# Kernel tuning notes

Hardware: AMD Instinct MI355X
Metric: run time of the kernel (lower is better)

The kernel has to match this reference:

```python
import jax, jax.numpy as jnp
import numpy as np


def _layernorm(x, g, b, eps=1e-5):
    mu = jnp.mean(x, axis=-1, keepdims=True)
    var = jnp.mean(jnp.square(x - mu), axis=-1, keepdims=True)
    return (x - mu) * jax.lax.rsqrt(var + eps) * g + b


def setup_inputs() -> dict:
    key = jax.random.key(0)
    ks = jax.random.split(key, 8)
    B, S, E, K, H = 32, 64, 768, 36, 4
    w = 0.02
    return {
        "x": jax.random.normal(ks[0], (B, S, E), dtype=jnp.float32),
        "y": jax.random.normal(ks[1], (B * S, K, E), dtype=jnp.float32),
        "ln_gamma": jnp.ones((H, E), jnp.float32),
        "ln_beta": jnp.zeros((H, E), jnp.float32),
        "W1": jax.random.normal(ks[2], (H, E, E), dtype=jnp.float32) * w,
        "b1": jnp.zeros((H, E), jnp.float32),
        "W2x": jax.random.normal(ks[3], (H, E), dtype=jnp.float32) * w,  # first half of Linear(2E,1)
        "W2y": jax.random.normal(ks[4], (H, E), dtype=jnp.float32) * w,  # second half of Linear(2E,1)
        "b2": jnp.zeros((H,), jnp.float32),
        "Wm": jax.random.normal(ks[5], (H * E, E), dtype=jnp.float32) * w,
        "bm": jnp.zeros((E,), jnp.float32),
        "select_indegree_num": 36,
    }


def reference(x, y, ln_gamma, ln_beta, W1, b1, W2x, W2y, b2, Wm, bm, select_indegree_num):
    # x: [B,S,E], y: [B*S,K,E]; dropout layers are identity in eval mode.
    B, S, E = x.shape
    H = ln_gamma.shape[0]
    xf = x.reshape(B * S, E)
    outs = []
    for h in range(H):
        # shared linear1 (LayerNorm + Linear) applied to both x and y
        x_ = _layernorm(xf, ln_gamma[h], ln_beta[h]) @ W1[h] + b1[h]          # [BS,E]
        y_ = _layernorm(y, ln_gamma[h], ln_beta[h]) @ W1[h] + b1[h]           # [BS,K,E]
        logit = (x_ @ W2x[h])[:, None] + y_ @ W2y[h] + b2[h]                  # [BS,K]
        prob = jax.nn.softmax(logit, axis=1)                                   # softmax over neighbors
        a = jnp.einsum('nk,nke->ne', prob, y_)                                 # weighted sum, [BS,E]
        outs.append(jax.nn.gelu(xf + a))                                       # GELU(x + a)
    cat = jnp.concatenate(outs, axis=-1)                                       # [BS,H*E]
    res = jax.nn.gelu(cat @ Wm + bm).reshape(B, S, E)
    return x + res  # has_residual=True
```

## Files before the change

kernel.cpp:

```cpp
#include <hip/hip_runtime.h>
#include <hip/hip_bf16.h>
#include <math.h>

#define EE 768
#define HH 4
#define KK 36
#define BSN 2048

typedef __attribute__((ext_vector_type(8))) short short8;
typedef __attribute__((ext_vector_type(4))) short short4v;
typedef __attribute__((ext_vector_type(4))) float float4v;

__device__ inline short f2bf(float x){
  return __builtin_bit_cast(short, __float2bfloat16(x));
}
__device__ inline float bf2f(short s){
  return __bfloat162float(__builtin_bit_cast(__hip_bfloat16, s));
}
__device__ inline float gelu_tanh(float x){
  float t = tanhf(0.79788456080286536f * (x + 0.044715f * x * x * x));
  return 0.5f * x * (1.0f + t);
}

__global__ __launch_bounds__(256) void k_v(const float* __restrict__ W1,
                                           const float* __restrict__ W2y,
                                           const float* __restrict__ g,
                                           const float* __restrict__ b1,
                                           float* __restrict__ v,
                                           float* __restrict__ b1p){
  const int wid  = blockIdx.x * 4 + (threadIdx.x >> 6);
  const int lane = threadIdx.x & 63;
  const int h = wid / EE, e = wid % EE;
  const float* W  = W1 + ((size_t)h * EE + e) * EE;
  const float* wy = W2y + h * EE;
  float acc = 0.f;
  #pragma unroll
  for (int j = 0; j < 12; ++j){
    int f = lane + 64 * j;
    acc += W[f] * wy[f];
  }
  #pragma unroll
  for (int off = 32; off; off >>= 1) acc += __shfl_xor(acc, off);
  if (lane == 0) v[h * EE + e] = g[h * EE + e] * acc;

  int idx = blockIdx.x * 256 + threadIdx.x;
  if (idx < HH * EE) b1p[idx] = b1[idx];
}

__global__ __launch_bounds__(256) void k_b1p_acc(const float* __restrict__ W1,
                                                 const float* __restrict__ beta,
                                                 float* __restrict__ b1p){
  const int h   = blockIdx.x >> 6;
  const int ec0 = (blockIdx.x & 63) * 12;
  const float* W  = W1 + (size_t)h * EE * EE;
  const float* bt = beta + h * EE;
  const int f = threadIdx.x;
  float a0 = 0.f, a1 = 0.f, a2 = 0.f;
  #pragma unroll
  for (int e = ec0; e < ec0 + 12; ++e){
    float be = bt[e];
    const float* row = W + (size_t)e * EE;
    a0 += be * row[f];
    a1 += be * row[f + 256];
    a2 += be * row[f + 512];
  }
  atomicAdd(&b1p[h * EE + f],       a0);
  atomicAdd(&b1p[h * EE + f + 256], a1);
  atomicAdd(&b1p[h * EE + f + 512], a2);
}

__global__ __launch_bounds__(256) void k_tW1(const float* __restrict__ W1,
                                             const float* __restrict__ g,
                                             short* __restrict__ W1t){
  __shared__ float tile[32][33];
  const int h  = blockIdx.z;
  const int e0 = blockIdx.x * 32, f0 = blockIdx.y * 32;
  const int tx = threadIdx.x & 31, ty = threadIdx.x >> 5;
  const float* W = W1 + (size_t)h * EE * EE;
  #pragma unroll
  for (int i = 0; i < 4; ++i){
    int e = e0 + ty + 8 * i;
    tile[ty + 8 * i][tx] = W[(size_t)e * EE + f0 + tx] * g[h * EE + e];
  }
  __syncthreads();
  #pragma unroll
  for (int i = 0; i < 4; ++i){
    int f = f0 + ty + 8 * i;
    W1t[((size_t)h * EE + f) * EE + e0 + tx] = f2bf(tile[tx][ty + 8 * i]);
  }
}

__global__ __launch_bounds__(256) void k_tWm(const float* __restrict__ Wm,
                                             short* __restrict__ Wmt){
  __shared__ float tile[32][33];
  const int c0 = blockIdx.x * 32, f0 = blockIdx.y * 32;
  const int tx = threadIdx.x & 31, ty = threadIdx.x >> 5;
  #pragma unroll
  for (int i = 0; i < 4; ++i){
    tile[ty + 8 * i][tx] = Wm[(size_t)(c0 + ty + 8 * i) * EE + f0 + tx];
  }
  __syncthreads();
  #pragma unroll
  for (int i = 0; i < 4; ++i){
    Wmt[(size_t)(f0 + ty + 8 * i) * (HH * EE) + c0 + tx] = f2bf(tile[tx][ty + 8 * i]);
  }
}

__global__ __launch_bounds__(256) void k_pass_y(const float* __restrict__ y,
                                                const float* __restrict__ v,
                                                short* __restrict__ p_y){
  const int wave = threadIdx.x >> 6, lane = threadIdx.x & 63;
  const int n = blockIdx.x * 4 + wave;
  const float* base = y + (size_t)n * KK * EE + 4 * lane;

  float4v vreg[HH][3];
  #pragma unroll
  for (int h = 0; h < HH; ++h)
    #pragma unroll
    for (int j = 0; j < 3; ++j)
      vreg[h][j] = *(const float4v*)(v + h * EE + 4 * lane + 256 * j);

  float4v acc[HH][3];
  #pragma unroll
  for (int h = 0; h < HH; ++h)
    #pragma unroll
    for (int j = 0; j < 3; ++j)
      acc[h][j] = (float4v){0.f, 0.f, 0.f, 0.f};
  float m[HH], l[HH];
  #pragma unroll
  for (int h = 0; h < HH; ++h){ m[h] = -INFINITY; l[h] = 0.f; }

  float4v bufA[3], bufB[3];
  #pragma unroll
  for (int j = 0; j < 3; ++j) bufA[j] = *(const float4v*)(base + 256 * j);
  #pragma unroll
  for (int j = 0; j < 3; ++j) bufB[j] = *(const float4v*)(base + EE + 256 * j);

  #pragma unroll 2
  for (int k = 0; k < KK; ++k){
    float4v cur[3];
    #pragma unroll
    for (int j = 0; j < 3; ++j) cur[j] = bufA[j];
    #pragma unroll
    for (int j = 0; j < 3; ++j) bufA[j] = bufB[j];
    if (k + 2 < KK){
      const float* rp = base + (size_t)(k + 2) * EE;
      #pragma unroll
      for (int j = 0; j < 3; ++j) bufB[j] = *(const float4v*)(rp + 256 * j);
    }

    float s = 0.f, s2 = 0.f;
    #pragma unroll
    for (int j = 0; j < 3; ++j)
      #pragma unroll
      for (int c = 0; c < 4; ++c){ float t = cur[j][c]; s += t; s2 += t * t; }
    #pragma unroll
    for (int off = 32; off; off >>= 1){
      s  += __shfl_xor(s, off);
      s2 += __shfl_xor(s2, off);
    }
    const float mu = s * (1.f / EE);
    const float rs = rsqrtf(s2 * (1.f / EE) - mu * mu + 1e-5f);

    float d[HH] = {0.f, 0.f, 0.f, 0.f};
    #pragma unroll
    for (int j = 0; j < 3; ++j)
      #pragma unroll
      for (int c = 0; c < 4; ++c){
        float t = (cur[j][c] - mu) * rs;
        cur[j][c] = t;
        d[0] += t * vreg[0][j][c];
        d[1] += t * vreg[1][j][c];
        d[2] += t * vreg[2][j][c];
        d[3] += t * vreg[3][j][c];
      }
    #pragma unroll
    for (int off = 32; off; off >>= 1){
      d[0] += __shfl_xor(d[0], off);
      d[1] += __shfl_xor(d[1], off);
      d[2] += __shfl_xor(d[2], off);
      d[3] += __shfl_xor(d[3], off);
    }

    #pragma unroll
    for (int h = 0; h < HH; ++h){
      if (d[h] > m[h]){
        float sc = __expf(m[h] - d[h]);
        l[h] *= sc;
        #pragma unroll
        for (int j = 0; j < 3; ++j)
          #pragma unroll
          for (int c = 0; c < 4; ++c) acc[h][j][c] *= sc;
        m[h] = d[h];
      }
      float w = __expf(d[h] - m[h]);
      l[h] += w;
      #pragma unroll
      for (int j = 0; j < 3; ++j)
        #pragma unroll
        for (int c = 0; c < 4; ++c) acc[h][j][c] += w * cur[j][c];
    }
  }

  #pragma unroll
  for (int h = 0; h < HH; ++h){
    const float inv = 1.f / l[h];
    #pragma unroll
    for (int j = 0; j < 3; ++j){
      short4v pk;
      #pragma unroll
      for (int c = 0; c < 4; ++c) pk[c] = f2bf(acc[h][j][c] * inv);
      *(short4v*)(p_y + ((size_t)h * BSN + n) * EE + 4 * lane + 256 * j) = pk;
    }
  }
}

template<int MODE>
__global__ __launch_bounds__(256) void k_gemm(const short* __restrict__ A,
                                              const short* __restrict__ Bt,
                                              const float* __restrict__ addv,
                                              const float* __restrict__ x,
                                              void* __restrict__ out,
                                              int Kdim, size_t strideA, size_t strideB){
  __shared__ short As[2][64][72];
  __shared__ short Bs[2][64][72];
  const int z = blockIdx.z;
  const short* Ah; const short* Bh; int kbeg, kend;
  if (MODE == 0){ Ah = A + strideA * z; Bh = Bt + strideB * z; kbeg = 0; kend = Kdim; }
  else          { Ah = A; Bh = Bt; kbeg = z * (Kdim >> 1); kend = kbeg + (Kdim >> 1); }

  const int tid = threadIdx.x;
  const int wave = tid >> 6, lane = tid & 63;
  const int quad = lane >> 4, l16 = lane & 15;
  const int m0 = blockIdx.x * 64, n0 = blockIdx.y * 64;
  const int r = tid >> 3, c8 = (tid & 7) * 8;

  float4v acc[4];
  #pragma unroll
  for (int t = 0; t < 4; ++t) acc[t] = (float4v){0.f, 0.f, 0.f, 0.f};

  const short* Ap0 = Ah + (size_t)(m0 + r) * Kdim + c8;
  const short* Ap1 = Ah + (size_t)(m0 + r + 32) * Kdim + c8;
  const short* Bp0 = Bh + (size_t)(n0 + r) * Kdim + c8;
  const short* Bp1 = Bh + (size_t)(n0 + r + 32) * Kdim + c8;

  short8 ra0 = *(const short8*)(Ap0 + kbeg);
  short8 ra1 = *(const short8*)(Ap1 + kbeg);
  short8 rb0 = *(const short8*)(Bp0 + kbeg);
  short8 rb1 = *(const short8*)(Bp1 + kbeg);
  *(short8*)(&As[0][r][c8])      = ra0;
  *(short8*)(&As[0][r + 32][c8]) = ra1;
  *(short8*)(&Bs[0][r][c8])      = rb0;
  *(short8*)(&Bs[0][r + 32][c8]) = rb1;
  if (kbeg + 64 < kend){
    ra0 = *(const short8*)(Ap0 + kbeg + 64);
    ra1 = *(const short8*)(Ap1 + kbeg + 64);
    rb0 = *(const short8*)(Bp0 + kbeg + 64);
    rb1 = *(const short8*)(Bp1 + kbeg + 64);
  }
  __syncthreads();

  int cur = 0;
  for (int k0 = kbeg; k0 < kend; k0 += 64){
    if (k0 + 64 < kend){
      const int nx = cur ^ 1;
      *(short8*)(&As[nx][r][c8])      = ra0;
      *(short8*)(&As[nx][r + 32][c8]) = ra1;
      *(short8*)(&Bs[nx][r][c8])      = rb0;
      *(short8*)(&Bs[nx][r + 32][c8]) = rb1;
      if (k0 + 128 < kend){
        ra0 = *(const short8*)(Ap0 + k0 + 128);
        ra1 = *(const short8*)(Ap1 + k0 + 128);
        rb0 = *(const short8*)(Bp0 + k0 + 128);
        rb1 = *(const short8*)(Bp1 + k0 + 128);
      }
    }
    #pragma unroll
    for (int kk = 0; kk < 64; kk += 32){
      short8 bf = *(const short8*)(&Bs[cur][16 * wave + l16][kk + quad * 8]);
      #pragma unroll
      for (int t = 0; t < 4; ++t){
        short8 af = *(const short8*)(&As[cur][16 * t + l16][kk + quad * 8]);
        acc[t] = __builtin_amdgcn_mfma_f32_16x16x32_bf16(af, bf, acc[t], 0, 0, 0);
      }
    }
    __syncthreads();
    cur ^= 1;
  }

  const int f = n0 + 16 * wave + l16;
  if (MODE == 0){
    const float add = addv[768 * z + f];
    #pragma unroll
    for (int t = 0; t < 4; ++t){
      #pragma unroll
      for (int rr = 0; rr < 4; ++rr){
        const int m = m0 + 16 * t + quad * 4 + rr;
        const float val = acc[t][rr] + add;
        const float xf = x[(size_t)m * EE + f];
        ((short*)out)[(size_t)m * (HH * EE) + 768 * z + f] = f2bf(gelu_tanh(xf + val));
      }
    }
  } else {
    float* po = (float*)out + (size_t)z * BSN * EE;
    #pragma unroll
    for (int t = 0; t < 4; ++t){
      #pragma unroll
      for (int rr = 0; rr < 4; ++rr){
        const int m = m0 + 16 * t + quad * 4 + rr;
        po[(size_t)m * EE + f] = acc[t][rr];
      }
    }
  }
}

__global__ __launch_bounds__(256) void k_ep(const float* __restrict__ part,
                                            const float* __restrict__ bm,
                                            const float* __restrict__ x,
                                            float* __restrict__ out){
  const size_t i = ((size_t)blockIdx.x * 256 + threadIdx.x) * 4;
  float4v p0 = *(const float4v*)(part + i);
  float4v p1 = *(const float4v*)(part + (size_t)BSN * EE + i);
  float4v xv = *(const float4v*)(x + i);
  float4v bv = *(const float4v*)(bm + (int)(i % EE));
  float4v o;
  #pragma unroll
  for (int c = 0; c < 4; ++c) o[c] = xv[c] + gelu_tanh(p0[c] + p1[c] + bv[c]);
  *(float4v*)(out + i) = o;
}

extern "C" void kernel_launch(void* const* d_in, const int* in_sizes, int n_in,
                              void* d_out, int out_size, void* d_ws, size_t ws_size,
                              hipStream_t stream){
  const float* x    = (const float*)d_in[0];
  const float* y    = (const float*)d_in[1];
  const float* g    = (const float*)d_in[2];
  const float* beta = (const float*)d_in[3];
  const float* W1   = (const float*)d_in[4];
  const float* b1   = (const float*)d_in[5];
  const float* W2y  = (const float*)d_in[7];
  const float* Wm   = (const float*)d_in[9];
  const float* bm   = (const float*)d_in[10];

  char* ws = (char*)d_ws;
  float* v    = (float*)(ws + 0);
  float* b1p  = (float*)(ws + 12288);
  short* W1t  = (short*)(ws + 24576);
  short* Wmt  = (short*)(ws + 4743168);
  short* p_y  = (short*)(ws + 9461760);
  short* catb = (short*)(ws + 22044672);
  float* part = (float*)(ws + 34627584);
  float* out  = (float*)d_out;

  k_v<<<dim3(768), dim3(256), 0, stream>>>(W1, W2y, g, b1, v, b1p);
  k_b1p_acc<<<dim3(256), dim3(256), 0, stream>>>(W1, beta, b1p);
  k_tW1<<<dim3(24, 24, 4), dim3(256), 0, stream>>>(W1, g, W1t);
  k_tWm<<<dim3(96, 24), dim3(256), 0, stream>>>(Wm, Wmt);
  k_pass_y<<<dim3(512), dim3(256), 0, stream>>>(y, v, p_y);
  k_gemm<0><<<dim3(32, 12, 4), dim3(256), 0, stream>>>(
      p_y, W1t, b1p, x, (void*)catb, 768, (size_t)2048 * 768, (size_t)768 * 768);
  k_gemm<1><<<dim3(32, 12, 2), dim3(256), 0, stream>>>(
      catb, Wmt, nullptr, nullptr, (void*)part, 3072, (size_t)0, (size_t)0);
  k_ep<<<dim3(1536), dim3(256), 0, stream>>>(part, bm, x, out);
}
```

Baseline: 427.4 us.

## Split neighbor softmax across two waves and fuse final epilogue into GEMM

```diff
diff --git a/kernel.cpp b/kernel.cpp
--- a/kernel.cpp
+++ b/kernel.cpp
@@ -109,9 +109,13 @@
 __global__ __launch_bounds__(256) void k_pass_y(const float* __restrict__ y,
                                                 const float* __restrict__ v,
                                                 short* __restrict__ p_y){
+  __shared__ float4v sacc[2][HH][3][64];
+  __shared__ float   sml[2][2][2][HH];
   const int wave = threadIdx.x >> 6, lane = threadIdx.x & 63;
-  const int n = blockIdx.x * 4 + wave;
-  const float* base = y + (size_t)n * KK * EE + 4 * lane;
+  const int row = wave >> 1, half = wave & 1;
+  const int n = blockIdx.x * 2 + row;
+  const int kh = 18;
+  const float* base = y + ((size_t)n * KK + half * kh) * EE + 4 * lane;
 
   float4v vreg[HH][3];
   #pragma unroll
@@ -137,13 +141,13 @@
   for (int j = 0; j < 3; ++j) bufB[j] = *(const float4v*)(base + EE + 256 * j);
 
   #pragma unroll 2
-  for (int k = 0; k < KK; ++k){
+  for (int k = 0; k < kh; ++k){
     float4v cur[3];
     #pragma unroll
     for (int j = 0; j < 3; ++j) cur[j] = bufA[j];
     #pragma unroll
     for (int j = 0; j < 3; ++j) bufA[j] = bufB[j];
-    if (k + 2 < KK){
+    if (k + 2 < kh){
       const float* rp = base + (size_t)(k + 2) * EE;
       #pragma unroll
       for (int j = 0; j < 3; ++j) bufB[j] = *(const float4v*)(rp + 256 * j);
@@ -202,15 +206,51 @@
     }
   }
 
+  if (lane == 0){
+    #pragma unroll
+    for (int h = 0; h < HH; ++h){
+      sml[row][half][0][h] = m[h];
+      sml[row][half][1][h] = l[h];
+    }
+  }
+  __syncthreads();
+
+  float escale[HH], L[HH];
   #pragma unroll
   for (int h = 0; h < HH; ++h){
-    const float inv = 1.f / l[h];
-    #pragma unroll
-    for (int j = 0; j < 3; ++j){
-      short4v pk;
-      #pragma unroll
-      for (int c = 0; c < 4; ++c) pk[c] = f2bf(acc[h][j][c] * inv);
-      *(short4v*)(p_y + ((size_t)h * BSN + n) * EE + 4 * lane + 256 * j) = pk;
+    const float mo = sml[row][half ^ 1][0][h];
+    const float lo = sml[row][half ^ 1][1][h];
+    const float M  = fmaxf(m[h], mo);
+    escale[h] = __expf(m[h] - M);
+    L[h] = l[h] * escale[h] + lo * __expf(mo - M);
+  }
+
+  if (half == 1){
+    #pragma unroll
+    for (int h = 0; h < HH; ++h)
+      #pragma unroll
+      for (int j = 0; j < 3; ++j){
+        float4v sv;
+        #pragma unroll
+        for (int c = 0; c < 4; ++c) sv[c] = acc[h][j][c] * escale[h];
+        sacc[row][h][j][lane] = sv;
+      }
+  }
+  __syncthreads();
+
+  if (half == 0){
+    #pragma unroll
+    for (int h = 0; h < HH; ++h){
+      const float inv = 1.f / L[h];
+      #pragma unroll
+      for (int j = 0; j < 3; ++j){
+        float4v ov = sacc[row][h][j][lane];
+        short4v pk;
+        #pragma unroll
+        for (int c = 0; c < 4; ++c)
+          pk[c] = f2bf((acc[h][j][c] * escale[h] + ov[c]) * inv);
+        *(short4v*)(p_y + ((size_t)h * BSN + n) * EE + 4 * lane + 256 * j) = pk;
+      }
     }
   }
 }
@@ -225,9 +265,9 @@
   __shared__ short As[2][64][72];
   __shared__ short Bs[2][64][72];
   const int z = blockIdx.z;
-  const short* Ah; const short* Bh; int kbeg, kend;
-  if (MODE == 0){ Ah = A + strideA * z; Bh = Bt + strideB * z; kbeg = 0; kend = Kdim; }
-  else          { Ah = A; Bh = Bt; kbeg = z * (Kdim >> 1); kend = kbeg + (Kdim >> 1); }
+  const short* Ah = A + strideA * z;
+  const short* Bh = Bt + strideB * z;
+  const int kbeg = 0, kend = Kdim;
 
   const int tid = threadIdx.x;
   const int wave = tid >> 6, lane = tid & 63;
@@ -302,31 +342,18 @@
       }
     }
   } else {
-    float* po = (float*)out + (size_t)z * BSN * EE;
+    const float add = addv[f];
+    float* po = (float*)out;
     #pragma unroll
     for (int t = 0; t < 4; ++t){
       #pragma unroll
       for (int rr = 0; rr < 4; ++rr){
         const int m = m0 + 16 * t + quad * 4 + rr;
-        po[(size_t)m * EE + f] = acc[t][rr];
-      }
-    }
-  }
-}
-
-__global__ __launch_bounds__(256) void k_ep(const float* __restrict__ part,
-                                            const float* __restrict__ bm,
-                                            const float* __restrict__ x,
-                                            float* __restrict__ out){
-  const size_t i = ((size_t)blockIdx.x * 256 + threadIdx.x) * 4;
-  float4v p0 = *(const float4v*)(part + i);
-  float4v p1 = *(const float4v*)(part + (size_t)BSN * EE + i);
-  float4v xv = *(const float4v*)(x + i);
-  float4v bv = *(const float4v*)(bm + (int)(i % EE));
-  float4v o;
-  #pragma unroll
-  for (int c = 0; c < 4; ++c) o[c] = xv[c] + gelu_tanh(p0[c] + p1[c] + bv[c]);
-  *(float4v*)(out + i) = o;
+        const float xf = x[(size_t)m * EE + f];
+        po[(size_t)m * EE + f] = xf + gelu_tanh(acc[t][rr] + add);
+      }
+    }
+  }
 }
 
 extern "C" void kernel_launch(void* const* d_in, const int* in_sizes, int n_in,
@@ -349,17 +376,15 @@
   short* Wmt  = (short*)(ws + 4743168);
   short* p_y  = (short*)(ws + 9461760);
   short* catb = (short*)(ws + 22044672);
-  float* part = (float*)(ws + 34627584);
   float* out  = (float*)d_out;
 
   k_v<<<dim3(768), dim3(256), 0, stream>>>(W1, W2y, g, b1, v, b1p);
   k_b1p_acc<<<dim3(256), dim3(256), 0, stream>>>(W1, beta, b1p);
   k_tW1<<<dim3(24, 24, 4), dim3(256), 0, stream>>>(W1, g, W1t);
   k_tWm<<<dim3(96, 24), dim3(256), 0, stream>>>(Wm, Wmt);
-  k_pass_y<<<dim3(512), dim3(256), 0, stream>>>(y, v, p_y);
+  k_pass_y<<<dim3(1024), dim3(256), 0, stream>>>(y, v, p_y);
   k_gemm<0><<<dim3(32, 12, 4), dim3(256), 0, stream>>>(
       p_y, W1t, b1p, x, (void*)catb, 768, (size_t)2048 * 768, (size_t)768 * 768);
-  k_gemm<1><<<dim3(32, 12, 2), dim3(256), 0, stream>>>(
-      catb, Wmt, nullptr, nullptr, (void*)part, 3072, (size_t)0, (size_t)0);
-  k_ep<<<dim3(1536), dim3(256), 0, stream>>>(part, bm, x, out);
-}
+  k_gemm<1><<<dim3(32, 12, 1), dim3(256), 0, stream>>>(
+      catb, Wmt, bm, x, (void*)out, 3072, (size_t)0, (size_t)0);
+}
```

Result: no change. 434.4 us (+1.6%).

## Merge weight-prep kernels and fuse final epilogue into unsplit output GEMM

Applied to the files above, without the earlier changes.

```diff
diff --git a/kernel.cpp b/kernel.cpp
--- a/kernel.cpp
+++ b/kernel.cpp
@@ -22,29 +22,68 @@
   return 0.5f * x * (1.0f + t);
 }
 
-__global__ __launch_bounds__(256) void k_v(const float* __restrict__ W1,
-                                           const float* __restrict__ W2y,
-                                           const float* __restrict__ g,
-                                           const float* __restrict__ b1,
-                                           float* __restrict__ v,
-                                           float* __restrict__ b1p){
-  const int wid  = blockIdx.x * 4 + (threadIdx.x >> 6);
-  const int lane = threadIdx.x & 63;
-  const int h = wid / EE, e = wid % EE;
-  const float* W  = W1 + ((size_t)h * EE + e) * EE;
-  const float* wy = W2y + h * EE;
-  float acc = 0.f;
-  #pragma unroll
-  for (int j = 0; j < 12; ++j){
-    int f = lane + 64 * j;
-    acc += W[f] * wy[f];
-  }
-  #pragma unroll
-  for (int off = 32; off; off >>= 1) acc += __shfl_xor(acc, off);
-  if (lane == 0) v[h * EE + e] = g[h * EE + e] * acc;
-
-  int idx = blockIdx.x * 256 + threadIdx.x;
-  if (idx < HH * EE) b1p[idx] = b1[idx];
+__global__ __launch_bounds__(256) void k_prep(const float* __restrict__ W1,
+                                              const float* __restrict__ W2y,
+                                              const float* __restrict__ g,
+                                              const float* __restrict__ b1,
+                                              const float* __restrict__ Wm,
+                                              float* __restrict__ v,
+                                              float* __restrict__ b1p,
+                                              short* __restrict__ W1t,
+                                              short* __restrict__ Wmt){
+  __shared__ float tile[32][33];
+  const int b = blockIdx.x;
+
+  if (b < 768){
+    const int wid  = b * 4 + (threadIdx.x >> 6);
+    const int lane = threadIdx.x & 63;
+    const int h = wid / EE, e = wid % EE;
+    const float* W  = W1 + ((size_t)h * EE + e) * EE;
+    const float* wy = W2y + h * EE;
+    float acc = 0.f;
+    #pragma unroll
+    for (int j = 0; j < 12; ++j){
+      int f = lane + 64 * j;
+      acc += W[f] * wy[f];
+    }
+    #pragma unroll
+    for (int off = 32; off; off >>= 1) acc += __shfl_xor(acc, off);
+    if (lane == 0) v[h * EE + e] = g[h * EE + e] * acc;
+
+    int idx = b * 256 + threadIdx.x;
+    if (idx < HH * EE) b1p[idx] = b1[idx];
+  } else if (b < 3072){
+    const int bb = b - 768;
+    const int et = bb % 24, ft = (bb / 24) % 24, h = bb / 576;
+    const int e0 = et * 32, f0 = ft * 32;
+    const int tx = threadIdx.x & 31, ty = threadIdx.x >> 5;
+    const float* W = W1 + (size_t)h * EE * EE;
+    #pragma unroll
+    for (int i = 0; i < 4; ++i){
+      int e = e0 + ty + 8 * i;
+      tile[ty + 8 * i][tx] = W[(size_t)e * EE + f0 + tx] * g[h * EE + e];
+    }
+    __syncthreads();
+    #pragma unroll
+    for (int i = 0; i < 4; ++i){
+      int f = f0 + ty + 8 * i;
+      W1t[((size_t)h * EE + f) * EE + e0 + tx] = f2bf(tile[tx][ty + 8 * i]);
+    }
+  } else {
+    const int bb = b - 3072;
+    const int ct = bb % 96, ft = bb / 96;
+    const int c0 = ct * 32, f0 = ft * 32;
+    const int tx = threadIdx.x & 31, ty = threadIdx.x >> 5;
+    #pragma unroll
+    for (int i = 0; i < 4; ++i){
+      tile[ty + 8 * i][tx] = Wm[(size_t)(c0 + ty + 8 * i) * EE + f0 + tx];
+    }
+    __syncthreads();
+    #pragma unroll
+    for (int i = 0; i < 4; ++i){
+      Wmt[(size_t)(f0 + ty + 8 * i) * (HH * EE) + c0 + tx] = f2bf(tile[tx][ty + 8 * i]);
+    }
+  }
 }
 
 __global__ __launch_bounds__(256) void k_b1p_acc(const float* __restrict__ W1,
@@ -67,43 +106,6 @@
   atomicAdd(&b1p[h * EE + f],       a0);
   atomicAdd(&b1p[h * EE + f + 256], a1);
   atomicAdd(&b1p[h * EE + f + 512], a2);
-}
-
-__global__ __launch_bounds__(256) void k_tW1(const float* __restrict__ W1,
-                                             const float* __restrict__ g,
-                                             short* __restrict__ W1t){
-  __shared__ float tile[32][33];
-  const int h  = blockIdx.z;
-  const int e0 = blockIdx.x * 32, f0 = blockIdx.y * 32;
-  const int tx = threadIdx.x & 31, ty = threadIdx.x >> 5;
-  const float* W = W1 + (size_t)h * EE * EE;
-  #pragma unroll
-  for (int i = 0; i < 4; ++i){
-    int e = e0 + ty + 8 * i;
-    tile[ty + 8 * i][tx] = W[(size_t)e * EE + f0 + tx] * g[h * EE + e];
-  }
-  __syncthreads();
-  #pragma unroll
-  for (int i = 0; i < 4; ++i){
-    int f = f0 + ty + 8 * i;
-    W1t[((size_t)h * EE + f) * EE + e0 + tx] = f2bf(tile[tx][ty + 8 * i]);
-  }
-}
-
-__global__ __launch_bounds__(256) void k_tWm(const float* __restrict__ Wm,
-                                             short* __restrict__ Wmt){
-  __shared__ float tile[32][33];
-  const int c0 = blockIdx.x * 32, f0 = blockIdx.y * 32;
-  const int tx = threadIdx.x & 31, ty = threadIdx.x >> 5;
-  #pragma unroll
-  for (int i = 0; i < 4; ++i){
-    tile[ty + 8 * i][tx] = Wm[(size_t)(c0 + ty + 8 * i) * EE + f0 + tx];
-  }
-  __syncthreads();
-  #pragma unroll
-  for (int i = 0; i < 4; ++i){
-    Wmt[(size_t)(f0 + ty + 8 * i) * (HH * EE) + c0 + tx] = f2bf(tile[tx][ty + 8 * i]);
-  }
 }
 
 __global__ __launch_bounds__(256) void k_pass_y(const float* __restrict__ y,
@@ -225,9 +227,9 @@
   __shared__ short As[2][64][72];
   __shared__ short Bs[2][64][72];
   const int z = blockIdx.z;
-  const short* Ah; const short* Bh; int kbeg, kend;
-  if (MODE == 0){ Ah = A + strideA * z; Bh = Bt + strideB * z; kbeg = 0; kend = Kdim; }
-  else          { Ah = A; Bh = Bt; kbeg = z * (Kdim >> 1); kend = kbeg + (Kdim >> 1); }
+  const short* Ah = A + strideA * z;
+  const short* Bh = Bt + strideB * z;
+  const int kbeg = 0, kend = Kdim;
 
   const int tid = threadIdx.x;
   const int wave = tid >> 6, lane = tid & 63;
@@ -302,31 +304,18 @@
       }
     }
   } else {
-    float* po = (float*)out + (size_t)z * BSN * EE;
+    const float add = addv[f];
+    float* po = (float*)out;
     #pragma unroll
     for (int t = 0; t < 4; ++t){
       #pragma unroll
       for (int rr = 0; rr < 4; ++rr){
         const int m = m0 + 16 * t + quad * 4 + rr;
-        po[(size_t)m * EE + f] = acc[t][rr];
-      }
-    }
-  }
-}
-
-__global__ __launch_bounds__(256) void k_ep(const float* __restrict__ part,
-                                            const float* __restrict__ bm,
-                                            const float* __restrict__ x,
-                                            float* __restrict__ out){
-  const size_t i = ((size_t)blockIdx.x * 256 + threadIdx.x) * 4;
-  float4v p0 = *(const float4v*)(part + i);
-  float4v p1 = *(const float4v*)(part + (size_t)BSN * EE + i);
-  float4v xv = *(const float4v*)(x + i);
-  float4v bv = *(const float4v*)(bm + (int)(i % EE));
-  float4v o;
-  #pragma unroll
-  for (int c = 0; c < 4; ++c) o[c] = xv[c] + gelu_tanh(p0[c] + p1[c] + bv[c]);
-  *(float4v*)(out + i) = o;
+        const float xf = x[(size_t)m * EE + f];
+        po[(size_t)m * EE + f] = xf + gelu_tanh(acc[t][rr] + add);
+      }
+    }
+  }
 }
 
 extern "C" void kernel_launch(void* const* d_in, const int* in_sizes, int n_in,
@@ -349,17 +338,13 @@
   short* Wmt  = (short*)(ws + 4743168);
   short* p_y  = (short*)(ws + 9461760);
   short* catb = (short*)(ws + 22044672);
-  float* part = (float*)(ws + 34627584);
   float* out  = (float*)d_out;
 
-  k_v<<<dim3(768), dim3(256), 0, stream>>>(W1, W2y, g, b1, v, b1p);
+  k_prep<<<dim3(5376), dim3(256), 0, stream>>>(W1, W2y, g, b1, Wm, v, b1p, W1t, Wmt);
   k_b1p_acc<<<dim3(256), dim3(256), 0, stream>>>(W1, beta, b1p);
-  k_tW1<<<dim3(24, 24, 4), dim3(256), 0, stream>>>(W1, g, W1t);
-  k_tWm<<<dim3(96, 24), dim3(256), 0, stream>>>(Wm, Wmt);
   k_pass_y<<<dim3(512), dim3(256), 0, stream>>>(y, v, p_y);
   k_gemm<0><<<dim3(32, 12, 4), dim3(256), 0, stream>>>(
       p_y, W1t, b1p, x, (void*)catb, 768, (size_t)2048 * 768, (size_t)768 * 768);
-  k_gemm<1><<<dim3(32, 12, 2), dim3(256), 0, stream>>>(
-      catb, Wmt, nullptr, nullptr, (void*)part, 3072, (size_t)0, (size_t)0);
-  k_ep<<<dim3(1536), dim3(256), 0, stream>>>(part, bm, x, out);
-}
+  k_gemm<1><<<dim3(32, 12, 1), dim3(256), 0, stream>>>(
+      catb, Wmt, bm, x, (void*)out, 3072, (size_t)0, (size_t)0);
+}
```

New measurement: 426.7 us, median of 2. About the same (-0.2%).
